# Kernel tuning notes

Measured on AMD Instinct MI355X. Metric: run time of the kernel, lower is better.

The kernel has to match this reference:

```python
import jax, jax.numpy as jnp
from jax import lax
import numpy as np

GRID, IMG, BLOCK = 60, 960, 16
BN_EPS = 1e-5


def _conv(x, w, b):
    return lax.conv_general_dilated(x, w, (1, 1), 'SAME', dimension_numbers=('NCHW', 'OIHW', 'NCHW')) + b[None, :, None, None]


def _bn(x, g, b):
    # inference BatchNorm with running_mean=0, running_var=1
    s = g * np.float32(1.0 / np.sqrt(1.0 + BN_EPS))
    return x * s[None, :, None, None] + b[None, :, None, None]


def _mlp(x, w1, b1, w2, b2):
    return jax.nn.relu(x @ w1.T + b1) @ w2.T + b2


def _lstm_layer(x, wih, whh, b):
    # x: [B,T,D]; torch gate order i,f,g,o; zero initial state
    B = x.shape[0]
    H = whh.shape[1]
    pre = jnp.swapaxes(x, 0, 1) @ wih.T + b  # [T,B,4H]

    def step(carry, p):
        h, c = carry
        z = p + h @ whh.T
        i, f, g, o = jnp.split(z, 4, axis=-1)
        c = jax.nn.sigmoid(f) * c + jax.nn.sigmoid(i) * jnp.tanh(g)
        h = jax.nn.sigmoid(o) * jnp.tanh(c)
        return (h, c), h

    z0 = jnp.zeros((B, H), x.dtype)
    (h, c), ys = lax.scan(step, (z0, z0), pre)
    return jnp.swapaxes(ys, 0, 1), h, c


def _forward(motion_vectors, boxes, track_ids, conv1_w, conv1_b, bn1_g, bn1_b, conv2_w, conv2_b, bn2_g, bn2_b, conv3_w, conv3_b, bn3_g, bn3_b, agg_w1, agg_b1, agg_w2, agg_b2, bx_w1, bx_b1, bx_w2, bx_b2, id_table, proj_w, proj_b, empty_slot, l0_wih, l0_whh, l0_b, l1_wih, l1_whh, l1_b, hb_w1, hb_b1, hb_w2, hb_b2, hc_w1, hc_b1, hc_w2, hc_b2, ht_w1, ht_b1, ht_w2, ht_b2):
    B = motion_vectors.shape[0]
    # ---- grid encoder (Conv-BN-ReLU x3) ----
    x = jax.nn.relu(_bn(_conv(motion_vectors, conv1_w, conv1_b), bn1_g, bn1_b))
    x = jax.nn.relu(_bn(_conv(x, conv2_w, conv2_b), bn2_g, bn2_b))
    gf = jax.nn.relu(_bn(_conv(x, conv3_w, conv3_b), bn3_g, bn3_b))  # [B,64,60,60]
    global_feat = gf.mean((-2, -1))  # AdaptiveAvgPool2d(1) -> [B,64]

    # ---- per-box motion statistics (vectorized masked reductions) ----
    bg = jnp.clip(boxes * (IMG / BLOCK), 0.0, GRID - 1e-6)  # grid coords
    ix1 = jnp.floor(bg[..., 0]); iy1 = jnp.floor(bg[..., 1])
    ix2 = jnp.maximum(ix1 + 1.0, jnp.ceil(bg[..., 2]))
    iy2 = jnp.maximum(iy1 + 1.0, jnp.ceil(bg[..., 3]))
    g = jnp.arange(GRID, dtype=bg.dtype)
    mx_ = (g >= ix1[..., None]) & (g < ix2[..., None])  # [B,N,60]
    my_ = (g >= iy1[..., None]) & (g < iy2[..., None])
    mask = my_[..., :, None] & mx_[..., None, :]  # [B,N,60,60]
    m = mask.astype(bg.dtype)
    cnt = m.sum((-2, -1))[..., None]  # [B,N,1], >= 1 by construction
    mv = motion_vectors  # [B,2,60,60]
    s1 = jnp.einsum('bnyx,bcyx->bnc', m, mv)
    s2 = jnp.einsum('bnyx,bcyx->bnc', m, mv * mv)
    mean = s1 / cnt
    var = (s2 - cnt * mean * mean) / jnp.maximum(cnt - 1.0, 1.0)  # unbiased, like torch .std()
    var_safe = jnp.where(cnt > 1.0, jnp.maximum(var, 1e-12), 1.0)
    std = jnp.where(cnt > 1.0, jnp.sqrt(var_safe), 0.0)
    BIG = jnp.asarray(1e9, bg.dtype)
    mn = jnp.min(jnp.where(mask[:, :, None], mv[:, None], BIG), axis=(-2, -1))   # [B,N,2]
    mx = jnp.max(jnp.where(mask[:, :, None], mv[:, None], -BIG), axis=(-2, -1))  # [B,N,2]
    stats = jnp.stack([mean[..., 0], mean[..., 1], std[..., 0], std[..., 1], mn[..., 0], mx[..., 0], mn[..., 1], mx[..., 1]], -1)  # [B,N,8]
    motion_emb = _mlp(stats, agg_w1, agg_b1, agg_w2, agg_b2)  # [B,N,64]

    # ---- slot initialization ----
    box_emb = _mlp(boxes, bx_w1, bx_b1, bx_w2, bx_b2)  # [B,N,64]
    id_emb = id_table[jnp.clip(track_ids, 0, 999)]  # [B,N,32]
    obj = jnp.concatenate([box_emb, id_emb, motion_emb], -1)  # [B,N,160]
    slots = obj @ proj_w.T + proj_b  # [B,300,128]; N == max_slots so no empty slots used

    # ---- 2-layer LSTM over the 300 slots (batch_first, eval -> no dropout) ----
    Ns = slots.shape[1]
    gexp = jnp.broadcast_to(global_feat[:, None, :], (B, Ns, global_feat.shape[-1]))
    lstm_in = jnp.concatenate([slots, gexp], -1)  # [B,300,192]
    y, h0, c0 = _lstm_layer(lstm_in, l0_wih, l0_whh, l0_b)
    y, h1, c1 = _lstm_layer(y, l1_wih, l1_whh, l1_b)  # [B,300,128]

    # ---- RT-DETR style heads ----
    pred_boxes = jax.nn.sigmoid(_mlp(y, hb_w1, hb_b1, hb_w2, hb_b2))  # [B,300,4]
    cls_logits = _mlp(y, hc_w1, hc_b1, hc_w2, hc_b2)  # [B,300,2]
    tid_logits = _mlp(y, ht_w1, ht_b1, ht_w2, ht_b2)  # [B,300,1000]
    h = jnp.stack([h0, h1])
    c = jnp.stack([c0, c1])
    return pred_boxes, cls_logits, tid_logits, h, c


def setup_inputs() -> dict:
    B, N = 32, 300
    key = jax.random.key(0)
    ks = iter(jax.random.split(key, 60))

    def w(*s):
        return jax.random.normal(next(ks), s, jnp.float32) * 0.05

    mv = jax.random.normal(next(ks), (B, 2, GRID, GRID), jnp.float32)
    bb = jax.random.uniform(next(ks), (B, N, 4), jnp.float32)
    boxes = jnp.concatenate([jnp.minimum(bb[..., :2], bb[..., 2:]), jnp.maximum(bb[..., :2], bb[..., 2:])], -1)
    track_ids = jax.random.randint(next(ks), (B, N), 0, 1000)
    return dict(
        motion_vectors=mv, boxes=boxes, track_ids=track_ids,
        conv1_w=w(32, 2, 3, 3), conv1_b=w(32), bn1_g=1.0 + w(32), bn1_b=w(32),
        conv2_w=w(64, 32, 3, 3), conv2_b=w(64), bn2_g=1.0 + w(64), bn2_b=w(64),
        conv3_w=w(64, 64, 3, 3), conv3_b=w(64), bn3_g=1.0 + w(64), bn3_b=w(64),
        agg_w1=w(32, 8), agg_b1=w(32), agg_w2=w(64, 32), agg_b2=w(64),
        bx_w1=w(32, 4), bx_b1=w(32), bx_w2=w(64, 32), bx_b2=w(64),
        id_table=w(1000, 32).at[0].set(0.0),
        proj_w=w(128, 160), proj_b=w(128), empty_slot=w(128),
        l0_wih=w(512, 192), l0_whh=w(512, 128), l0_b=w(512),
        l1_wih=w(512, 128), l1_whh=w(512, 128), l1_b=w(512),
        hb_w1=w(256, 128), hb_b1=w(256), hb_w2=w(4, 256), hb_b2=w(4),
        hc_w1=w(256, 128), hc_b1=w(256), hc_w2=w(2, 256), hc_b2=w(2),
        ht_w1=w(256, 128), ht_b1=w(256), ht_w2=w(1000, 256), ht_b2=w(1000))


def reference(motion_vectors, boxes, track_ids, conv1_w, conv1_b, bn1_g, bn1_b, conv2_w, conv2_b, bn2_g, bn2_b, conv3_w, conv3_b, bn3_g, bn3_b, agg_w1, agg_b1, agg_w2, agg_b2, bx_w1, bx_b1, bx_w2, bx_b2, id_table, proj_w, proj_b, empty_slot, l0_wih, l0_whh, l0_b, l1_wih, l1_whh, l1_b, hb_w1, hb_b1, hb_w2, hb_b2, hc_w1, hc_b1, hc_w2, hc_b2, ht_w1, ht_b1, ht_w2, ht_b2):
    return _forward(motion_vectors, boxes, track_ids, conv1_w, conv1_b, bn1_g, bn1_b, conv2_w, conv2_b, bn2_g, bn2_b, conv3_w, conv3_b, bn3_g, bn3_b, agg_w1, agg_b1, agg_w2, agg_b2, bx_w1, bx_b1, bx_w2, bx_b2, id_table, proj_w, proj_b, empty_slot, l0_wih, l0_whh, l0_b, l1_wih, l1_whh, l1_b, hb_w1, hb_b1, hb_w2, hb_b2, hc_w1, hc_b1, hc_w2, hc_b2, ht_w1, ht_b1, ht_w2, ht_b2)
```

## Files before the change

### kernel.cpp

```cpp
#include <hip/hip_runtime.h>
#include <hip/hip_bf16.h>
#include <math.h>

typedef unsigned short ushort_t;
typedef __attribute__((ext_vector_type(8))) short bf16x8;
typedef __attribute__((ext_vector_type(4))) float f32x4;

__device__ __forceinline__ float sigf(float x) {
  x = fminf(fmaxf(x, -30.f), 30.f);
  return 1.f / (1.f + __expf(-x));
}
__device__ __forceinline__ float sig2(float x) {
  return __builtin_amdgcn_rcpf(1.f + __expf(-x));
}
__device__ __forceinline__ float tanh2(float x) {
  return 1.f - 2.f * __builtin_amdgcn_rcpf(__expf(2.f * x) + 1.f);
}
__device__ __forceinline__ ushort_t f2bf(float x) {
  unsigned int b = __float_as_uint(x);
  unsigned int lsb = (b >> 16) & 1u;
  b += 0x7fffu + lsb;
  return (ushort_t)(b >> 16);
}
__device__ __forceinline__ float bf2f(ushort_t u) {
  return __uint_as_float(((unsigned int)u) << 16);
}

#define NPIX 3600
__device__ __forceinline__ int gperm(int rho) {
  return ((rho & 3) << 7) + (rho >> 2);
}

__global__ __launch_bounds__(256) void wprep_kernel(
    const float* __restrict__ conv2_w, const float* __restrict__ conv3_w,
    const float* __restrict__ wih0,
    const float* __restrict__ projW,
    const float* __restrict__ projb,
    const float* __restrict__ l0_b,
    const float* __restrict__ hbw1, const float* __restrict__ hcw1,
    const float* __restrict__ htw1, const float* __restrict__ htw2,
    const float* __restrict__ hbb1, const float* __restrict__ hcb1,
    const float* __restrict__ htb1, ushort_t* __restrict__ wc2,
    ushort_t* __restrict__ wc3, ushort_t* __restrict__ wAp,
    float* __restrict__ l0bp, ushort_t* __restrict__ whid,
    ushort_t* __restrict__ wt2, float* __restrict__ bhid) {
  int i = blockIdx.x * 256 + threadIdx.x;
  if (i < 18432) {
    int oc = i / 288, r = i % 288, kt = r / 32, ic = r % 32;
    wc2[i] = f2bf(conv2_w[((oc * 32 + ic) * 3 + kt / 3) * 3 + kt % 3]);
    return;
  }
  i -= 18432;
  if (i < 36864) {
    int oc = i / 576, r = i % 576, c = r / 288, r2 = r % 288;
    int kt = r2 / 32, icl = r2 % 32, ic = c * 32 + icl;
    wc3[i] = f2bf(conv3_w[((oc * 64 + ic) * 3 + kt / 3) * 3 + kt % 3]);
    return;
  }
  i -= 36864;
  if (i < 98304) {
    int n = i / 192, k = i % 192;
    int src = gperm(n);
    float a = 0.f;
    if (k < 160) {
      const float* wr = wih0 + src * 192;
      for (int j = 0; j < 128; ++j) a = fmaf(wr[j], projW[j * 160 + k], a);
    }
    wAp[i] = f2bf(a);
    return;
  }
  i -= 98304;
  if (i < 512) {
    int src = gperm(i);
    float a = l0_b[src];
    const float* wr = wih0 + src * 192;
    for (int j = 0; j < 128; ++j) a = fmaf(wr[j], projb[j], a);
    l0bp[i] = a;
    return;
  }
  i -= 512;
  if (i < 98304) {
    int row = i >> 7, c = i & 127;
    float v = (row < 256)   ? hbw1[row * 128 + c]
              : (row < 512) ? hcw1[(row - 256) * 128 + c]
                            : htw1[(row - 512) * 128 + c];
    whid[i] = f2bf(v);
    return;
  }
  i -= 98304;
  if (i < 256000) {
    wt2[i] = f2bf(htw2[i]);
    return;
  }
  i -= 256000;
  if (i < 768)
    bhid[i] = (i < 256) ? hbb1[i] : (i < 512) ? hcb1[i - 256] : htb1[i - 512];
}

__global__ __launch_bounds__(256) void gvec_kernel(
    const float* __restrict__ wih0, const float* __restrict__ gf,
    float* __restrict__ gvec) {
  int i = blockIdx.x * 256 + threadIdx.x;
  int b = i >> 9, n = i & 511;
  const float* wr = wih0 + gperm(n) * 192 + 128;
  const float* g = gf + b * 64;
  float a = 0.f;
#pragma unroll
  for (int k = 0; k < 64; ++k) a = fmaf(wr[k], g[k], a);
  gvec[i] = a * (1.f / 3600.f);
}

__global__ __launch_bounds__(256) void front_kernel(
    const float* __restrict__ mv, const float* __restrict__ c1w,
    const float* __restrict__ c1b, const float* __restrict__ bg1,
    const float* __restrict__ bb1, ushort_t* __restrict__ x1out,
    const float* __restrict__ boxes, const int* __restrict__ ids,
    const float* __restrict__ agg_w1, const float* __restrict__ agg_b1,
    const float* __restrict__ agg_w2, const float* __restrict__ agg_b2,
    const float* __restrict__ bx_w1, const float* __restrict__ bx_b1,
    const float* __restrict__ bx_w2, const float* __restrict__ bx_b2,
    const float* __restrict__ id_table, ushort_t* __restrict__ obj_out) {
  if (blockIdx.x < 14400) {
    int idx = blockIdx.x * 256 + threadIdx.x;
    int x = idx % 60;
    int y = (idx / 60) % 60;
    int oc = (idx / 3600) % 32;
    int b = idx / (3600 * 32);
    float acc = 0.f;
#pragma unroll
    for (int ic = 0; ic < 2; ++ic) {
      const float* src = mv + (b * 2 + ic) * NPIX;
      const float* wp = c1w + (oc * 2 + ic) * 9;
#pragma unroll
      for (int ky = 0; ky < 3; ++ky) {
        int gy = y + ky - 1;
        if (gy < 0 || gy >= 60) continue;
#pragma unroll
        for (int kx = 0; kx < 3; ++kx) {
          int gx = x + kx - 1;
          if (gx < 0 || gx >= 60) continue;
          acc = fmaf(src[gy * 60 + gx], wp[ky * 3 + kx], acc);
        }
      }
    }
    float s = bg1[oc] * rsqrtf(1.f + 1e-5f);
    float v = fmaf(acc, s, fmaf(c1b[oc], s, bb1[oc]));
    x1out[idx] = f2bf(fmaxf(v, 0.f));
    return;
  }
  __shared__ float obj[2][160];
  __shared__ float hm[2][32];
  __shared__ float hbx[2][32];
  __shared__ float stats[2][8];
  __shared__ float boxf[2][4];
  __shared__ float red[2][2][8];
  int h = threadIdx.x >> 7;
  int t = threadIdx.x & 127;
  int blk = (blockIdx.x - 14400) * 2 + h;
  int b = blk / 300;
  float bx0 = boxes[blk * 4 + 0], by0 = boxes[blk * 4 + 1];
  float bx1 = boxes[blk * 4 + 2], by1 = boxes[blk * 4 + 3];
  const float HI = (float)(60.0 - 1e-6);
  float gx1 = fminf(fmaxf(bx0 * 60.f, 0.f), HI);
  float gy1 = fminf(fmaxf(by0 * 60.f, 0.f), HI);
  float gx2 = fminf(fmaxf(bx1 * 60.f, 0.f), HI);
  float gy2 = fminf(fmaxf(by1 * 60.f, 0.f), HI);
  float fx1 = floorf(gx1), fy1 = floorf(gy1);
  float fx2 = fmaxf(fx1 + 1.f, ceilf(gx2));
  float fy2 = fmaxf(fy1 + 1.f, ceilf(gy2));
  int ix1 = (int)fx1, iy1 = (int)fy1, ix2 = (int)fx2, iy2 = (int)fy2;
  int w = ix2 - ix1, hgt = iy2 - iy1;
  int area = w * hgt;
  float s0 = 0.f, s1 = 0.f, q0 = 0.f, q1 = 0.f;
  float mn0 = 1e9f, mn1 = 1e9f, mx0 = -1e9f, mx1 = -1e9f;
  const float* mv0 = mv + b * 2 * NPIX;
  const float* mv1 = mv0 + NPIX;
  for (int i = t; i < area; i += 128) {
    int r = i / w, cc = i - r * w;
    int yy = iy1 + r, xx = ix1 + cc;
    float v0 = mv0[yy * 60 + xx];
    float v1 = mv1[yy * 60 + xx];
    s0 += v0; q0 += v0 * v0; mn0 = fminf(mn0, v0); mx0 = fmaxf(mx0, v0);
    s1 += v1; q1 += v1 * v1; mn1 = fminf(mn1, v1); mx1 = fmaxf(mx1, v1);
  }
#pragma unroll
  for (int off = 32; off; off >>= 1) {
    s0 += __shfl_down(s0, off); s1 += __shfl_down(s1, off);
    q0 += __shfl_down(q0, off); q1 += __shfl_down(q1, off);
    mn0 = fminf(mn0, __shfl_down(mn0, off));
    mn1 = fminf(mn1, __shfl_down(mn1, off));
    mx0 = fmaxf(mx0, __shfl_down(mx0, off));
    mx1 = fmaxf(mx1, __shfl_down(mx1, off));
// ... 179 lines not shown
    }
#pragma unroll
    for (int q = 0; q < 2; ++q) {
      int idx = q * 256 + tid;
      int row = idx >> 3, ch = idx & 7;
      int n = n0 + row;
      uint4 v = make_uint4(0, 0, 0, 0);
      if (n < N) v = *(const uint4*)(W + (size_t)n * K + kc * 64 + ch * 8);
      *(uint4*)(&Ws[row * 64 + ((ch * 8) ^ ((row & 7) << 3))]) = v;
    }
    __syncthreads();
#pragma unroll
    for (int ks = 0; ks < 2; ++ks) {
      bf16x8 bfr[2], afr[4];
#pragma unroll
      for (int ni = 0; ni < 2; ++ni) {
        int row = wn * 32 + ni * 16 + col;
        bfr[ni] = *(const bf16x8*)(
            &Ws[row * 64 + ((ks * 32 + kg * 8) ^ ((row & 7) << 3))]);
      }
#pragma unroll
      for (int mi = 0; mi < 4; ++mi) {
        int row = wm * 64 + mi * 16 + col;
        afr[mi] = *(const bf16x8*)(
            &As[row * 64 + ((ks * 32 + kg * 8) ^ ((row & 7) << 3))]);
      }
#pragma unroll
      for (int mi = 0; mi < 4; ++mi)
#pragma unroll
        for (int ni = 0; ni < 2; ++ni)
          acc[mi][ni] = __builtin_amdgcn_mfma_f32_16x16x32_bf16(
              afr[mi], bfr[ni], acc[mi][ni], 0, 0, 0);
    }
  }
#pragma unroll
  for (int ni = 0; ni < 2; ++ni) {
    int n = n0 + wn * 32 + ni * 16 + col;
    float bn = (n < N) ? bias[n] : 0.f;
#pragma unroll
    for (int mi = 0; mi < 4; ++mi) {
      int mbase = m0 + wm * 64 + mi * 16 + kg * 4;
#pragma unroll
      for (int r = 0; r < 4; ++r) {
        float v = acc[mi][ni][r] + bn;
        if (GVEC) v += gvec[((mbase + r) / 300) * 512 + n];
        if (ACT == 1) v = fmaxf(v, 0.f);
        if (n < N) {
          if (OBF16)
            ((ushort_t*)C)[(size_t)(mbase + r) * ldc + n] = f2bf(v);
          else
            ((float*)C)[(size_t)(mbase + r) * ldc + n] = v;
        }
      }
    }
  }
}

__global__ __launch_bounds__(256) void head_small_kernel(
    const ushort_t* __restrict__ hid, const float* __restrict__ wb2,
    const float* __restrict__ bb2, const float* __restrict__ wc2,
    const float* __restrict__ bc2, float* __restrict__ outB,
    float* __restrict__ outC) {
  int idx = blockIdx.x * 256 + threadIdx.x;
  int row = idx / 6, j = idx % 6;
  const ushort_t* h = hid + (size_t)row * 768 + (j < 4 ? 0 : 256);
  const float* wrow = (j < 4) ? wb2 + j * 256 : wc2 + (j - 4) * 256;
  float acc = (j < 4) ? bb2[j] : bc2[j - 4];
  for (int k = 0; k < 256; k += 8) {
    uint4 hv = *(const uint4*)(h + k);
    unsigned int ww[4] = {hv.x, hv.y, hv.z, hv.w};
#pragma unroll
    for (int q = 0; q < 4; ++q) {
      acc = fmaf(bf2f((ushort_t)(ww[q] & 0xffff)), wrow[k + 2 * q], acc);
      acc = fmaf(bf2f((ushort_t)(ww[q] >> 16)), wrow[k + 2 * q + 1], acc);
    }
  }
  float v = (j < 4) ? sigf(acc) : acc;
  if (j < 4) outB[row * 4 + j] = v;
  else outC[row * 2 + (j - 4)] = v;
}

#define LSTM_BAR() asm volatile("s_waitcnt lgkmcnt(0)\n\ts_barrier" ::: "memory")

__global__ __launch_bounds__(512) void lstm_fused_kernel(
    const float* __restrict__ pre0,
    const float* __restrict__ whh0,
    const float* __restrict__ wih1,
    const float* __restrict__ whh1,
    const float* __restrict__ b1,
    float* __restrict__ pre1,
    ushort_t* __restrict__ y0,
    ushort_t* __restrict__ y1,
    float* __restrict__ outH, float* __restrict__ outC,
    unsigned int* __restrict__ flags)
{
  __shared__ ushort_t h_lds[2][4][160];
  int tid = threadIdx.x;
  int w = tid >> 6, lane = tid & 63;
  int col = lane & 15, kg = lane >> 4;
  int bat = col & 3, q = col >> 2;
  int cell = (4 * w + q) * 4 + kg;

  if (blockIdx.x < 8) {
    int g = blockIdx.x;
    int b0 = g * 4;
    unsigned int* flagp = &flags[g * 32];
    for (int i = tid; i < 2 * 4 * 160; i += 512) ((ushort_t*)h_lds)[i] = 0;
    bf16x8 aW0[4][4];
#pragma unroll
    for (int j = 0; j < 4; ++j) {
      int rho = (4 * w + j) * 16 + col;
      int src = gperm(rho);
#pragma unroll
      for (int kt = 0; kt < 4; ++kt) {
        const float* s1 = whh0 + src * 128 + kt * 32 + kg * 8;
        bf16x8 f1;
#pragma unroll
        for (int qq = 0; qq < 8; ++qq) f1[qq] = (short)f2bf(s1[qq]);
        aW0[j][kt] = f1;
      }
    }
    const float* pg = pre0 + (size_t)(b0 + bat) * 300 * 512 + 4 * cell;
    ushort_t* yg0 = y0 + ((size_t)(b0 + bat) * 300) * 128 + cell;
    float c = 0.f, hout = 0.f;
    f32x4 p0v = *(const f32x4*)(pg);
    f32x4 p1v = *(const f32x4*)(pg + 512);
    __syncthreads();

    for (int s = 0; s < 300; ++s) {
      const ushort_t* hb = h_lds[s & 1][bat];
      bf16x8 bfr[4];
#pragma unroll
      for (int kt = 0; kt < 4; ++kt)
        bfr[kt] = *(const bf16x8*)(hb + kt * 32 + kg * 8);
      f32x4 a0 = {0.f, 0.f, 0.f, 0.f}, a1 = a0, a2 = a0, a3 = a0;
#pragma unroll
      for (int kt = 0; kt < 4; ++kt) {
        a0 = __builtin_amdgcn_mfma_f32_16x16x32_bf16(aW0[0][kt], bfr[kt], a0, 0, 0, 0);
        a1 = __builtin_amdgcn_mfma_f32_16x16x32_bf16(aW0[1][kt], bfr[kt], a1, 0, 0, 0);
        a2 = __builtin_amdgcn_mfma_f32_16x16x32_bf16(aW0[2][kt], bfr[kt], a2, 0, 0, 0);
        a3 = __builtin_amdgcn_mfma_f32_16x16x32_bf16(aW0[3][kt], bfr[kt], a3, 0, 0, 0);
      }
      f32x4 z = a0;
      if (q == 1) z = a1;
      if (q == 2) z = a2;
      if (q == 3) z = a3;
      {
        float zi = z[0] + p0v[0];
        float zf = z[1] + p0v[1];
        float zg = z[2] + p0v[2];
        float zo = z[3] + p0v[3];
        float vi = sig2(zi), vf = sig2(zf), vg = tanh2(zg), vo = sig2(zo);
        c = vf * c + vi * vg;
        hout = vo * tanh2(c);
        ushort_t hv = f2bf(hout);
        h_lds[(s + 1) & 1][bat][cell] = hv;
        __builtin_nontemporal_store(hv, yg0 + (size_t)s * 128);
        p0v = p1v;
        int sn = (s + 2 < 300) ? s + 2 : 299;
        p1v = *(const f32x4*)(pg + (size_t)sn * 512);
      }
      asm volatile("s_waitcnt vmcnt(6)" ::: "memory");
      LSTM_BAR();
      if (tid == 0 && s >= 3)
        __hip_atomic_store(flagp, (unsigned int)(s - 3), __ATOMIC_RELAXED,
                           __HIP_MEMORY_SCOPE_AGENT);
    }
    asm volatile("s_waitcnt vmcnt(0)" ::: "memory");
    __syncthreads();
    if (tid == 0)
      __hip_atomic_store(flagp, 300u, __ATOMIC_RELAXED,
                         __HIP_MEMORY_SCOPE_AGENT);
    outH[(b0 + bat) * 128 + cell] = hout;
    outC[(b0 + bat) * 128 + cell] = c;
  } else if (blockIdx.x < 16) {
    int g = blockIdx.x - 8;
    int b0 = g * 4;
    unsigned int* flagp = &flags[g * 32 + 16];
    for (int i = tid; i < 2 * 4 * 160; i += 512) ((ushort_t*)h_lds)[i] = 0;
    bf16x8 aW[4][4];
#pragma unroll
    for (int j = 0; j < 4; ++j) {
      int rho = (4 * w + j) * 16 + col;
      int src = gperm(rho);
#pragma unroll
      for (int kt = 0; kt < 4; ++kt) {
        const float* s1 = whh1 + src * 128 + kt * 32 + kg * 8;
        bf16x8 f1;
#pragma unroll
        for (int qq = 0; qq < 8; ++qq) f1[qq] = (short)f2bf(s1[qq]);
        aW[j][kt] = f1;
      }
    }
    float bi = b1[cell], bff = b1[128 + cell], bgg = b1[256 + cell],
          boo = b1[384 + cell];
    const float* pg = pre1 + (size_t)(b0 + bat) * 300 * 512 + 4 * cell;
    ushort_t* yg = y1 + (size_t)(b0 + bat) * 300 * 128 + cell;
    float c = 0.f, hout = 0.f;
    unsigned int fc = 0;
    f32x4 p0v, p1v;
    do {
      fc = __hip_atomic_load(flagp, __ATOMIC_RELAXED,
                             __HIP_MEMORY_SCOPE_AGENT);
      if (fc < 1) __builtin_amdgcn_s_sleep(2);
    } while (fc < 1);
    asm volatile("" ::: "memory");
    p0v = __builtin_nontemporal_load((const f32x4*)(pg));
    while (fc < 2) {
      fc = __hip_atomic_load(flagp, __ATOMIC_RELAXED,
                             __HIP_MEMORY_SCOPE_AGENT);
      if (fc < 2) __builtin_amdgcn_s_sleep(2);
    }
    asm volatile("" ::: "memory");
    p1v = __builtin_nontemporal_load((const f32x4*)(pg + 512));
    __syncthreads();

    for (int t = 0; t < 300; ++t) {
      const ushort_t* hb = h_lds[t & 1][bat];
      bf16x8 bfr[4];
#pragma unroll
      for (int kt = 0; kt < 4; ++kt)
        bfr[kt] = *(const bf16x8*)(hb + kt * 32 + kg * 8);
      f32x4 a0 = {0.f, 0.f, 0.f, 0.f}, a1 = a0, a2 = a0, a3 = a0;
#pragma unroll
      for (int kt = 0; kt < 4; ++kt) {
        a0 = __builtin_amdgcn_mfma_f32_16x16x32_bf16(aW[0][kt], bfr[kt], a0, 0, 0, 0);
        a1 = __builtin_amdgcn_mfma_f32_16x16x32_bf16(aW[1][kt], bfr[kt], a1, 0, 0, 0);
        a2 = __builtin_amdgcn_mfma_f32_16x16x32_bf16(aW[2][kt], bfr[kt], a2, 0, 0, 0);
        a3 = __builtin_amdgcn_mfma_f32_16x16x32_bf16(aW[3][kt], bfr[kt], a3, 0, 0, 0);
      }
      f32x4 z = a0;
      if (q == 1) z = a1;
      if (q == 2) z = a2;
      if (q == 3) z = a3;
      {
        float zi = z[0] + p0v[0] + bi;
        float zf = z[1] + p0v[1] + bff;
        float zg = z[2] + p0v[2] + bgg;
        float zo = z[3] + p0v[3] + boo;
        float vi = sig2(zi), vf = sig2(zf), vg = tanh2(zg), vo = sig2(zo);
        c = vf * c + vi * vg;
        hout = vo * tanh2(c);
        ushort_t hv = f2bf(hout);
        h_lds[(t + 1) & 1][bat][cell] = hv;
        yg[(size_t)t * 128] = hv;
        p0v = p1v;
        if (t + 2 < 300) {
          unsigned int need = (unsigned int)(t + 3);
          if (fc < need) {
            do {
              fc = __hip_atomic_load(flagp, __ATOMIC_RELAXED,
                                     __HIP_MEMORY_SCOPE_AGENT);
              if (fc < need) __builtin_amdgcn_s_sleep(2);
            } while (fc < need);
            asm volatile("" ::: "memory");
          }
          p1v = __builtin_nontemporal_load(
              (const f32x4*)(pg + (size_t)(t + 2) * 512));
        }
      }
      LSTM_BAR();
    }
    outH[4096 + (b0 + bat) * 128 + cell] = hout;
    outC[4096 + (b0 + bat) * 128 + cell] = c;
  } else {
    int g = blockIdx.x - 16;
    int b0 = g * 4;
    unsigned int* flag0 = &flags[g * 32];
    unsigned int* flag1 = &flags[g * 32 + 16];
    bf16x8 aU[4][4];
#pragma unroll
    for (int j = 0; j < 4; ++j) {
      int rho = (4 * w + j) * 16 + col;
      int src = gperm(rho);
#pragma unroll
      for (int kt = 0; kt < 4; ++kt) {
        const float* s2 = wih1 + src * 128 + kt * 32 + kg * 8;
        bf16x8 f2;
#pragma unroll
        for (int qq = 0; qq < 8; ++qq) f2[qq] = (short)f2bf(s2[qq]);
        aU[j][kt] = f2;
      }
    }
    int bb = col & 3;
    int ts = col >> 2;
    const ushort_t* yb = y0 + ((size_t)(b0 + bb) * 300) * 128 + kg * 8;
    unsigned int fc = 0;
    for (int t0 = 0; t0 < 300; t0 += 12) {
      unsigned int need = (unsigned int)(t0 + 11);
      while (fc < need) {
        fc = __hip_atomic_load(flag0, __ATOMIC_RELAXED,
                               __HIP_MEMORY_SCOPE_AGENT);
        if (fc < need) __builtin_amdgcn_s_sleep(2);
      }
      asm volatile("" ::: "memory");
      f32x4 acc[4][3];
#pragma unroll
      for (int j = 0; j < 4; ++j)
#pragma unroll
        for (int ct = 0; ct < 3; ++ct) acc[j][ct] = (f32x4){0.f, 0.f, 0.f, 0.f};
#pragma unroll
      for (int ct = 0; ct < 3; ++ct) {
        int t = t0 + ct * 4 + ts;
        bf16x8 bfr[4];
#pragma unroll
        for (int kt = 0; kt < 4; ++kt)
          bfr[kt] = __builtin_nontemporal_load(
              (const bf16x8*)(yb + (size_t)t * 128 + kt * 32));
#pragma unroll
        for (int kt = 0; kt < 4; ++kt) {
          acc[0][ct] = __builtin_amdgcn_mfma_f32_16x16x32_bf16(aU[0][kt], bfr[kt], acc[0][ct], 0, 0, 0);
          acc[1][ct] = __builtin_amdgcn_mfma_f32_16x16x32_bf16(aU[1][kt], bfr[kt], acc[1][ct], 0, 0, 0);
          acc[2][ct] = __builtin_amdgcn_mfma_f32_16x16x32_bf16(aU[2][kt], bfr[kt], acc[2][ct], 0, 0, 0);
          acc[3][ct] = __builtin_amdgcn_mfma_f32_16x16x32_bf16(aU[3][kt], bfr[kt], acc[3][ct], 0, 0, 0);
        }
      }
#pragma unroll
      for (int ct = 0; ct < 3; ++ct) {
        int t = t0 + ct * 4 + ts;
        float* pd = pre1 + ((size_t)(b0 + bb) * 300 + t) * 512 + kg * 4;
#pragma unroll
        for (int j = 0; j < 4; ++j)
          __builtin_nontemporal_store(acc[j][ct],
                                      (f32x4*)(pd + (4 * w + j) * 16));
      }
      asm volatile("s_waitcnt vmcnt(0)" ::: "memory");
      __syncthreads();
      if (tid == 0)
        __hip_atomic_store(flag1, (unsigned int)(t0 + 12), __ATOMIC_RELAXED,
                           __HIP_MEMORY_SCOPE_AGENT);
    }
  }
}

extern "C" void kernel_launch(void* const* d_in, const int* in_sizes, int n_in,
                              void* d_out, int out_size, void* d_ws,
                              size_t ws_size, hipStream_t stream) {
  const float* mv = (const float*)d_in[0];
  const float* boxes = (const float*)d_in[1];
  const int* track_ids = (const int*)d_in[2];
  const float* conv1_w = (const float*)d_in[3];
  const float* conv1_b = (const float*)d_in[4];
  const float* bn1_g = (const float*)d_in[5];
  const float* bn1_b = (const float*)d_in[6];
  const float* conv2_w = (const float*)d_in[7];
  const float* conv2_b = (const float*)d_in[8];
  const float* bn2_g = (const float*)d_in[9];
  const float* bn2_b = (const float*)d_in[10];
  const float* conv3_w = (const float*)d_in[11];
  const float* conv3_b = (const float*)d_in[12];
  const float* bn3_g = (const float*)d_in[13];
  const float* bn3_b = (const float*)d_in[14];
  const float* agg_w1 = (const float*)d_in[15];
  const float* agg_b1 = (const float*)d_in[16];
  const float* agg_w2 = (const float*)d_in[17];
  const float* agg_b2 = (const float*)d_in[18];
  const float* bx_w1 = (const float*)d_in[19];
  const float* bx_b1 = (const float*)d_in[20];
  const float* bx_w2 = (const float*)d_in[21];
  const float* bx_b2 = (const float*)d_in[22];
  const float* id_table = (const float*)d_in[23];
  const float* proj_w = (const float*)d_in[24];
  const float* proj_b = (const float*)d_in[25];
  const float* l0_wih = (const float*)d_in[27];
  const float* l0_whh = (const float*)d_in[28];
  const float* l0_b = (const float*)d_in[29];
  const float* l1_wih = (const float*)d_in[30];
  const float* l1_whh = (const float*)d_in[31];
  const float* l1_b = (const float*)d_in[32];
  const float* hb_w1 = (const float*)d_in[33];
  const float* hb_b1 = (const float*)d_in[34];
  const float* hb_w2 = (const float*)d_in[35];
  const float* hb_b2 = (const float*)d_in[36];
  const float* hc_w1 = (const float*)d_in[37];
  const float* hc_b1 = (const float*)d_in[38];
  const float* hc_w2 = (const float*)d_in[39];
  const float* hc_b2 = (const float*)d_in[40];
  const float* ht_w1 = (const float*)d_in[41];
  const float* ht_b1 = (const float*)d_in[42];
  const float* ht_w2 = (const float*)d_in[43];
  const float* ht_b2 = (const float*)d_in[44];

  char* wsb = (char*)d_ws;
  ushort_t* x1u = (ushort_t*)(wsb + 0);
  ushort_t* x2u = (ushort_t*)(wsb + 7372800);
  float* pre0 = (float*)(wsb + 0);
  ushort_t* hid = (ushort_t*)(wsb + 0);
  ushort_t* y0g = (ushort_t*)(wsb + 19660800);
  float* gf = (float*)(wsb + 22118400);
  ushort_t* obj = (ushort_t*)(wsb + 22126592);
  float* pre1 = (float*)(wsb + 25812992);
  ushort_t* y1b = (ushort_t*)(wsb + 45473792);
  unsigned int* flags = (unsigned int*)(wsb + 47931392);
  ushort_t* wAp = (ushort_t*)(wsb + 47932416);
  ushort_t* whid = (ushort_t*)(wsb + 48129024);
  ushort_t* wt2 = (ushort_t*)(wsb + 48325632);
  float* bhid = (float*)(wsb + 48837632);
  float* l0bp = (float*)(wsb + 48840704);
  float* gvec = (float*)(wsb + 48842752);
  ushort_t* wc2 = (ushort_t*)(wsb + 48908288);
  ushort_t* wc3 = (ushort_t*)(wsb + 48945152);

  float* outB = (float*)d_out;
  float* outC = outB + 38400;
  float* outT = outB + 57600;
  float* outH = outB + 9657600;
  float* outCc = outB + 9665792;

  hipMemsetAsync(gf, 0, 2048 * sizeof(float), stream);
  hipMemsetAsync(flags, 0, 1024, stream);

  wprep_kernel<<<1989, 256, 0, stream>>>(
      conv2_w, conv3_w, l0_wih, proj_w, proj_b, l0_b, hb_w1, hc_w1, ht_w1,
      ht_w2, hb_b1, hc_b1, ht_b1, wc2, wc3, wAp, l0bp, whid, wt2, bhid);
  front_kernel<<<19200, 256, 0, stream>>>(
      mv, conv1_w, conv1_b, bn1_g, bn1_b, x1u, boxes, track_ids, agg_w1,
      agg_b1, agg_w2, agg_b2, bx_w1, bx_b1, bx_w2, bx_b2, id_table, obj);
  conv_mfma_kernel<32, false><<<dim3(16, 32), 256, 0, stream>>>(
      x1u, wc2, conv2_b, bn2_g, bn2_b, x2u, nullptr);
  conv_mfma_kernel<64, true><<<dim3(16, 32), 256, 0, stream>>>(
      x2u, wc3, conv3_b, bn3_g, bn3_b, nullptr, gf);
  gvec_kernel<<<64, 256, 0, stream>>>(l0_wih, gf, gvec);
  gemm_bf16w_kernel<0, false, true><<<dim3(75, 8), 256, 0, stream>>>(
      obj, 192, wAp, l0bp, pre0, 512, 9600, 512, 192, gvec);
  lstm_fused_kernel<<<24, 512, 0, stream>>>(pre0, l0_whh, l1_wih, l1_whh,
                                            l1_b, pre1, y0g, y1b, outH, outCc,
                                            flags);
  gemm_bf16w_kernel<1, true, false><<<dim3(75, 12), 256, 0, stream>>>(
      y1b, 128, whid, bhid, hid, 768, 9600, 768, 128, nullptr);
  head_small_kernel<<<225, 256, 0, stream>>>(hid, hb_w2, hb_b2, hc_w2, hc_b2,
                                             outB, outC);
  gemm_bf16w_kernel<0, false, false><<<dim3(75, 16), 256, 0, stream>>>(
      hid + 512, 768, wt2, ht_b2, outT, 1000, 9600, 1000, 256, nullptr);
}
```

Baseline: 535.5 us.

## Halve LSTM block to four waves with two cells per lane and exp2-prescaled gates

The fused LSTM kernel now runs 256 threads per block instead of 512. Each wave holds 8 gate-weight tiles and each lane updates two hidden cells, so the per-step barrier spans fewer waves. Gate pre-activations are pre-multiplied by log2(e), or 2·log2(e) for the g gate, in the weight prep, bias and gvec kernels and in the recurrent weights, which lets the activations use exp2 directly without a multiply. In exchange each wave carries twice the register load and issues twice the MFMAs serially per step, which could lengthen the recurrent critical path.

```diff
diff --git a/kernel.cpp b/kernel.cpp
--- a/kernel.cpp
+++ b/kernel.cpp
@@ -6,15 +6,11 @@
 typedef __attribute__((ext_vector_type(8))) short bf16x8;
 typedef __attribute__((ext_vector_type(4))) float f32x4;
 
+#define LOG2E 1.4426950408889634f
+
 __device__ __forceinline__ float sigf(float x) {
   x = fminf(fmaxf(x, -30.f), 30.f);
   return 1.f / (1.f + __expf(-x));
-}
-__device__ __forceinline__ float sig2(float x) {
-  return __builtin_amdgcn_rcpf(1.f + __expf(-x));
-}
-__device__ __forceinline__ float tanh2(float x) {
-  return 1.f - 2.f * __builtin_amdgcn_rcpf(__expf(2.f * x) + 1.f);
 }
 __device__ __forceinline__ ushort_t f2bf(float x) {
   unsigned int b = __float_as_uint(x);
@@ -24,6 +20,9 @@
 }
 __device__ __forceinline__ float bf2f(ushort_t u) {
   return __uint_as_float(((unsigned int)u) << 16);
+}
+__device__ __forceinline__ float gsc(int g3) {
+  return (g3 == 2) ? (2.f * LOG2E) : LOG2E;
 }
 
 #define NPIX 3600
@@ -66,7 +65,7 @@
       const float* wr = wih0 + src * 192;
       for (int j = 0; j < 128; ++j) a = fmaf(wr[j], projW[j * 160 + k], a);
     }
-    wAp[i] = f2bf(a);
+    wAp[i] = f2bf(a * gsc(n & 3));
     return;
   }
   i -= 98304;
@@ -75,7 +74,7 @@
     float a = l0_b[src];
     const float* wr = wih0 + src * 192;
     for (int j = 0; j < 128; ++j) a = fmaf(wr[j], projb[j], a);
-    l0bp[i] = a;
+    l0bp[i] = a * gsc(i & 3);
     return;
   }
   i -= 512;
@@ -107,7 +106,7 @@
   float a = 0.f;
 #pragma unroll
   for (int k = 0; k < 64; ++k) a = fmaf(wr[k], g[k], a);
-  gvec[i] = a * (1.f / 3600.f);
+  gvec[i] = a * (1.f / 3600.f) * gsc(n & 3);
 }
 
 __global__ __launch_bounds__(256) void front_kernel(
@@ -453,7 +452,7 @@
 
 #define LSTM_BAR() asm volatile("s_waitcnt lgkmcnt(0)\n\ts_barrier" ::: "memory")
 
-__global__ __launch_bounds__(512) void lstm_fused_kernel(
+__global__ __launch_bounds__(256, 1) void lstm_fused_kernel(
     const float* __restrict__ pre0,
     const float* __restrict__ whh0,
     const float* __restrict__ wih1,
@@ -470,32 +469,38 @@
   int w = tid >> 6, lane = tid & 63;
   int col = lane & 15, kg = lane >> 4;
   int bat = col & 3, q = col >> 2;
-  int cell = (4 * w + q) * 4 + kg;
+  int cellA = 32 * w + 4 * q + kg;
+  int cellB = cellA + 16;
+  float wsc = gsc(col & 3);
 
   if (blockIdx.x < 8) {
     int g = blockIdx.x;
     int b0 = g * 4;
     unsigned int* flagp = &flags[g * 32];
-    for (int i = tid; i < 2 * 4 * 160; i += 512) ((ushort_t*)h_lds)[i] = 0;
-    bf16x8 aW0[4][4];
-#pragma unroll
-    for (int j = 0; j < 4; ++j) {
-      int rho = (4 * w + j) * 16 + col;
+    for (int i = tid; i < 2 * 4 * 160; i += 256) ((ushort_t*)h_lds)[i] = 0;
+    bf16x8 aW0[8][4];
+#pragma unroll
+    for (int j = 0; j < 8; ++j) {
+      int rho = (8 * w + j) * 16 + col;
       int src = gperm(rho);
 #pragma unroll
       for (int kt = 0; kt < 4; ++kt) {
         const float* s1 = whh0 + src * 128 + kt * 32 + kg * 8;
         bf16x8 f1;
 #pragma unroll
-        for (int qq = 0; qq < 8; ++qq) f1[qq] = (short)f2bf(s1[qq]);
+        for (int qq = 0; qq < 8; ++qq) f1[qq] = (short)f2bf(s1[qq] * wsc);
         aW0[j][kt] = f1;
       }
     }
-    const float* pg = pre0 + (size_t)(b0 + bat) * 300 * 512 + 4 * cell;
-    ushort_t* yg0 = y0 + ((size_t)(b0 + bat) * 300) * 128 + cell;
-    float c = 0.f, hout = 0.f;
-    f32x4 p0v = *(const f32x4*)(pg);
-    f32x4 p1v = *(const f32x4*)(pg + 512);
+    const float* pgA = pre0 + (size_t)(b0 + bat) * 300 * 512 + 4 * cellA;
+    const float* pgB = pgA + 64;
+    ushort_t* ygA = y0 + ((size_t)(b0 + bat) * 300) * 128 + cellA;
+    ushort_t* ygB = ygA + 16;
+    float cA = 0.f, cB = 0.f, hA = 0.f, hB = 0.f;
+    f32x4 p0A = *(const f32x4*)(pgA);
+    f32x4 p0B = *(const f32x4*)(pgB);
+    f32x4 p1A = *(const f32x4*)(pgA + 512);
+    f32x4 p1B = *(const f32x4*)(pgB + 512);
     __syncthreads();
 
     for (int s = 0; s < 300; ++s) {
@@ -504,34 +509,61 @@
 #pragma unroll
       for (int kt = 0; kt < 4; ++kt)
         bfr[kt] = *(const bf16x8*)(hb + kt * 32 + kg * 8);
-      f32x4 a0 = {0.f, 0.f, 0.f, 0.f}, a1 = a0, a2 = a0, a3 = a0;
+      f32x4 ac0 = {0.f, 0.f, 0.f, 0.f}, ac1 = ac0, ac2 = ac0, ac3 = ac0;
+      f32x4 ac4 = ac0, ac5 = ac0, ac6 = ac0, ac7 = ac0;
 #pragma unroll
       for (int kt = 0; kt < 4; ++kt) {
-        a0 = __builtin_amdgcn_mfma_f32_16x16x32_bf16(aW0[0][kt], bfr[kt], a0, 0, 0, 0);
-        a1 = __builtin_amdgcn_mfma_f32_16x16x32_bf16(aW0[1][kt], bfr[kt], a1, 0, 0, 0);
-        a2 = __builtin_amdgcn_mfma_f32_16x16x32_bf16(aW0[2][kt], bfr[kt], a2, 0, 0, 0);
-        a3 = __builtin_amdgcn_mfma_f32_16x16x32_bf16(aW0[3][kt], bfr[kt], a3, 0, 0, 0);
-      }
-      f32x4 z = a0;
-      if (q == 1) z = a1;
-      if (q == 2) z = a2;
-      if (q == 3) z = a3;
+        ac0 = __builtin_amdgcn_mfma_f32_16x16x32_bf16(aW0[0][kt], bfr[kt], ac0, 0, 0, 0);
+        ac1 = __builtin_amdgcn_mfma_f32_16x16x32_bf16(aW0[1][kt], bfr[kt], ac1, 0, 0, 0);
+        ac2 = __builtin_amdgcn_mfma_f32_16x16x32_bf16(aW0[2][kt], bfr[kt], ac2, 0, 0, 0);
+        ac3 = __builtin_amdgcn_mfma_f32_16x16x32_bf16(aW0[3][kt], bfr[kt], ac3, 0, 0, 0);
+        ac4 = __builtin_amdgcn_mfma_f32_16x16x32_bf16(aW0[4][kt], bfr[kt], ac4, 0, 0, 0);
+        ac5 = __builtin_amdgcn_mfma_f32_16x16x32_bf16(aW0[5][kt], bfr[kt], ac5, 0, 0, 0);
+        ac6 = __builtin_amdgcn_mfma_f32_16x16x32_bf16(aW0[6][kt], bfr[kt], ac6, 0, 0, 0);
+        ac7 = __builtin_amdgcn_mfma_f32_16x16x32_bf16(aW0[7][kt], bfr[kt], ac7, 0, 0, 0);
+      }
+      f32x4 zA = ac0;
+      if (q == 1) zA = ac1;
+      if (q == 2) zA = ac2;
+      if (q == 3) zA = ac3;
+      f32x4 zB = ac4;
+      if (q == 1) zB = ac5;
+      if (q == 2) zB = ac6;
+      if (q == 3) zB = ac7;
       {
-        float zi = z[0] + p0v[0];
-        float zf = z[1] + p0v[1];
-        float zg = z[2] + p0v[2];
-        float zo = z[3] + p0v[3];
-        float vi = sig2(zi), vf = sig2(zf), vg = tanh2(zg), vo = sig2(zo);
-        c = vf * c + vi * vg;
-        hout = vo * tanh2(c);
-        ushort_t hv = f2bf(hout);
-        h_lds[(s + 1) & 1][bat][cell] = hv;
-        __builtin_nontemporal_store(hv, yg0 + (size_t)s * 128);
-        p0v = p1v;
-        int sn = (s + 2 < 300) ? s + 2 : 299;
-        p1v = *(const f32x4*)(pg + (size_t)sn * 512);
-      }
-      asm volatile("s_waitcnt vmcnt(6)" ::: "memory");
+        float zi = zA[0] + p0A[0], zf = zA[1] + p0A[1];
+        float zg = zA[2] + p0A[2], zo = zA[3] + p0A[3];
+        float vi = __builtin_amdgcn_rcpf(1.f + __builtin_amdgcn_exp2f(-zi));
+        float vf = __builtin_amdgcn_rcpf(1.f + __builtin_amdgcn_exp2f(-zf));
+        float vg = 1.f - 2.f * __builtin_amdgcn_rcpf(__builtin_amdgcn_exp2f(zg) + 1.f);
+        float vo = __builtin_amdgcn_rcpf(1.f + __builtin_amdgcn_exp2f(-zo));
+        cA = vf * cA + vi * vg;
+        hA = vo * (1.f - 2.f * __builtin_amdgcn_rcpf(
+                             __builtin_amdgcn_exp2f(2.f * LOG2E * cA) + 1.f));
+        ushort_t hv = f2bf(hA);
+        h_lds[(s + 1) & 1][bat][cellA] = hv;
+        __builtin_nontemporal_store(hv, ygA + (size_t)s * 128);
+      }
+      {
+        float zi = zB[0] + p0B[0], zf = zB[1] + p0B[1];
+        float zg = zB[2] + p0B[2], zo = zB[3] + p0B[3];
+        float vi = __builtin_amdgcn_rcpf(1.f + __builtin_amdgcn_exp2f(-zi));
+        float vf = __builtin_amdgcn_rcpf(1.f + __builtin_amdgcn_exp2f(-zf));
+        float vg = 1.f - 2.f * __builtin_amdgcn_rcpf(__builtin_amdgcn_exp2f(zg) + 1.f);
+        float vo = __builtin_amdgcn_rcpf(1.f + __builtin_amdgcn_exp2f(-zo));
+        cB = vf * cB + vi * vg;
+        hB = vo * (1.f - 2.f * __builtin_amdgcn_rcpf(
+                             __builtin_amdgcn_exp2f(2.f * LOG2E * cB) + 1.f));
+        ushort_t hv = f2bf(hB);
+        h_lds[(s + 1) & 1][bat][cellB] = hv;
+        __builtin_nontemporal_store(hv, ygB + (size_t)s * 128);
+      }
+      p0A = p1A;
+      p0B = p1B;
+      int sn = (s + 2 < 300) ? s + 2 : 299;
+      p1A = *(const f32x4*)(pgA + (size_t)sn * 512);
+      p1B = *(const f32x4*)(pgB + (size_t)sn * 512);
+      asm volatile("s_waitcnt vmcnt(12)" ::: "memory");
       LSTM_BAR();
       if (tid == 0 && s >= 3)
         __hip_atomic_store(flagp, (unsigned int)(s - 3), __ATOMIC_RELAXED,
@@ -542,48 +574,56 @@
     if (tid == 0)
       __hip_atomic_store(flagp, 300u, __ATOMIC_RELAXED,
                          __HIP_MEMORY_SCOPE_AGENT);
-    outH[(b0 + bat) * 128 + cell] = hout;
-    outC[(b0 + bat) * 128 + cell] = c;
+    outH[(b0 + bat) * 128 + cellA] = hA;
+    outH[(b0 + bat) * 128 + cellB] = hB;
+    outC[(b0 + bat) * 128 + cellA] = cA;
+    outC[(b0 + bat) * 128 + cellB] = cB;
   } else if (blockIdx.x < 16) {
     int g = blockIdx.x - 8;
     int b0 = g * 4;
     unsigned int* flagp = &flags[g * 32 + 16];
-    for (int i = tid; i < 2 * 4 * 160; i += 512) ((ushort_t*)h_lds)[i] = 0;
-    bf16x8 aW[4][4];
-#pragma unroll
-    for (int j = 0; j < 4; ++j) {
-      int rho = (4 * w + j) * 16 + col;
+    for (int i = tid; i < 2 * 4 * 160; i += 256) ((ushort_t*)h_lds)[i] = 0;
+    bf16x8 aW[8][4];
+#pragma unroll
+    for (int j = 0; j < 8; ++j) {
+      int rho = (8 * w + j) * 16 + col;
       int src = gperm(rho);
 #pragma unroll
       for (int kt = 0; kt < 4; ++kt) {
         const float* s1 = whh1 + src * 128 + kt * 32 + kg * 8;
         bf16x8 f1;
 #pragma unroll
-        for (int qq = 0; qq < 8; ++qq) f1[qq] = (short)f2bf(s1[qq]);
+        for (int qq = 0; qq < 8; ++qq) f1[qq] = (short)f2bf(s1[qq] * wsc);
         aW[j][kt] = f1;
       }
     }
-    float bi = b1[cell], bff = b1[128 + cell], bgg = b1[256 + cell],
-          boo = b1[384 + cell];
-    const float* pg = pre1 + (size_t)(b0 + bat) * 300 * 512 + 4 * cell;
-    ushort_t* yg = y1 + (size_t)(b0 + bat) * 300 * 128 + cell;
-    float c = 0.f, hout = 0.f;
+    float biA = b1[cellA] * LOG2E, bfA = b1[128 + cellA] * LOG2E;
+    float bgA = b1[256 + cellA] * (2.f * LOG2E), boA = b1[384 + cellA] * LOG2E;
+    float biB = b1[cellB] * LOG2E, bfB = b1[128 + cellB] * LOG2E;
+    float bgB = b1[256 + cellB] * (2.f * LOG2E), boB = b1[384 + cellB] * LOG2E;
+    const float* pgA = pre1 + (size_t)(b0 + bat) * 300 * 512 + 4 * cellA;
+    const float* pgB = pgA + 64;
+    ushort_t* ygA = y1 + (size_t)(b0 + bat) * 300 * 128 + cellA;
+    ushort_t* ygB = ygA + 16;
+    float cA = 0.f, cB = 0.f, hA = 0.f, hB = 0.f;
     unsigned int fc = 0;
-    f32x4 p0v, p1v;
+    f32x4 p0A, p0B, p1A, p1B;
     do {
       fc = __hip_atomic_load(flagp, __ATOMIC_RELAXED,
                              __HIP_MEMORY_SCOPE_AGENT);
       if (fc < 1) __builtin_amdgcn_s_sleep(2);
     } while (fc < 1);
     asm volatile("" ::: "memory");
-    p0v = __builtin_nontemporal_load((const f32x4*)(pg));
+    p0A = __builtin_nontemporal_load((const f32x4*)(pgA));
+    p0B = __builtin_nontemporal_load((const f32x4*)(pgB));
     while (fc < 2) {
       fc = __hip_atomic_load(flagp, __ATOMIC_RELAXED,
                              __HIP_MEMORY_SCOPE_AGENT);
       if (fc < 2) __builtin_amdgcn_s_sleep(2);
     }
     asm volatile("" ::: "memory");
-    p1v = __builtin_nontemporal_load((const f32x4*)(pg + 512));
+    p1A = __builtin_nontemporal_load((const f32x4*)(pgA + 512));
+    p1B = __builtin_nontemporal_load((const f32x4*)(pgB + 512));
     __syncthreads();
 
     for (int t = 0; t < 300; ++t) {
@@ -592,64 +632,94 @@
 #pragma unroll
       for (int kt = 0; kt < 4; ++kt)
         bfr[kt] = *(const bf16x8*)(hb + kt * 32 + kg * 8);
-      f32x4 a0 = {0.f, 0.f, 0.f, 0.f}, a1 = a0, a2 = a0, a3 = a0;
+      f32x4 ac0 = {0.f, 0.f, 0.f, 0.f}, ac1 = ac0, ac2 = ac0, ac3 = ac0;
+      f32x4 ac4 = ac0, ac5 = ac0, ac6 = ac0, ac7 = ac0;
 #pragma unroll
       for (int kt = 0; kt < 4; ++kt) {
-        a0 = __builtin_amdgcn_mfma_f32_16x16x32_bf16(aW[0][kt], bfr[kt], a0, 0, 0, 0);
-        a1 = __builtin_amdgcn_mfma_f32_16x16x32_bf16(aW[1][kt], bfr[kt], a1, 0, 0, 0);
-        a2 = __builtin_amdgcn_mfma_f32_16x16x32_bf16(aW[2][kt], bfr[kt], a2, 0, 0, 0);
-        a3 = __builtin_amdgcn_mfma_f32_16x16x32_bf16(aW[3][kt], bfr[kt], a3, 0, 0, 0);
-      }
-      f32x4 z = a0;
-      if (q == 1) z = a1;
-      if (q == 2) z = a2;
-      if (q == 3) z = a3;
+        ac0 = __builtin_amdgcn_mfma_f32_16x16x32_bf16(aW[0][kt], bfr[kt], ac0, 0, 0, 0);
+        ac1 = __builtin_amdgcn_mfma_f32_16x16x32_bf16(aW[1][kt], bfr[kt], ac1, 0, 0, 0);
+        ac2 = __builtin_amdgcn_mfma_f32_16x16x32_bf16(aW[2][kt], bfr[kt], ac2, 0, 0, 0);
+        ac3 = __builtin_amdgcn_mfma_f32_16x16x32_bf16(aW[3][kt], bfr[kt], ac3, 0, 0, 0);
+        ac4 = __builtin_amdgcn_mfma_f32_16x16x32_bf16(aW[4][kt], bfr[kt], ac4, 0, 0, 0);
+        ac5 = __builtin_amdgcn_mfma_f32_16x16x32_bf16(aW[5][kt], bfr[kt], ac5, 0, 0, 0);
+        ac6 = __builtin_amdgcn_mfma_f32_16x16x32_bf16(aW[6][kt], bfr[kt], ac6, 0, 0, 0);
+        ac7 = __builtin_amdgcn_mfma_f32_16x16x32_bf16(aW[7][kt], bfr[kt], ac7, 0, 0, 0);
+      }
+      f32x4 zA = ac0;
+      if (q == 1) zA = ac1;
+      if (q == 2) zA = ac2;
+      if (q == 3) zA = ac3;
+      f32x4 zB = ac4;
+      if (q == 1) zB = ac5;
+      if (q == 2) zB = ac6;
+      if (q == 3) zB = ac7;
       {
-        float zi = z[0] + p0v[0] + bi;
-        float zf = z[1] + p0v[1] + bff;
-        float zg = z[2] + p0v[2] + bgg;
-        float zo = z[3] + p0v[3] + boo;
-        float vi = sig2(zi), vf = sig2(zf), vg = tanh2(zg), vo = sig2(zo);
-        c = vf * c + vi * vg;
-        hout = vo * tanh2(c);
-        ushort_t hv = f2bf(hout);
-        h_lds[(t + 1) & 1][bat][cell] = hv;
-        yg[(size_t)t * 128] = hv;
-        p0v = p1v;
-        if (t + 2 < 300) {
-          unsigned int need = (unsigned int)(t + 3);
-          if (fc < need) {
-            do {
-              fc = __hip_atomic_load(flagp, __ATOMIC_RELAXED,
-                                     __HIP_MEMORY_SCOPE_AGENT);
-              if (fc < need) __builtin_amdgcn_s_sleep(2);
-            } while (fc < need);
-            asm volatile("" ::: "memory");
-          }
-          p1v = __builtin_nontemporal_load(
-              (const f32x4*)(pg + (size_t)(t + 2) * 512));
+        float zi = zA[0] + p0A[0] + biA, zf = zA[1] + p0A[1] + bfA;
+        float zg = zA[2] + p0A[2] + bgA, zo = zA[3] + p0A[3] + boA;
+        float vi = __builtin_amdgcn_rcpf(1.f + __builtin_amdgcn_exp2f(-zi));
+        float vf = __builtin_amdgcn_rcpf(1.f + __builtin_amdgcn_exp2f(-zf));
+        float vg = 1.f - 2.f * __builtin_amdgcn_rcpf(__builtin_amdgcn_exp2f(zg) + 1.f);
+        float vo = __builtin_amdgcn_rcpf(1.f + __builtin_amdgcn_exp2f(-zo));
+        cA = vf * cA + vi * vg;
+        hA = vo * (1.f - 2.f * __builtin_amdgcn_rcpf(
+                             __builtin_amdgcn_exp2f(2.f * LOG2E * cA) + 1.f));
+        ushort_t hv = f2bf(hA);
+        h_lds[(t + 1) & 1][bat][cellA] = hv;
+        ygA[(size_t)t * 128] = hv;
+      }
+      {
+        float zi = zB[0] + p0B[0] + biB, zf = zB[1] + p0B[1] + bfB;
+        float zg = zB[2] + p0B[2] + bgB, zo = zB[3] + p0B[3] + boB;
+        float vi = __builtin_amdgcn_rcpf(1.f + __builtin_amdgcn_exp2f(-zi));
+        float vf = __builtin_amdgcn_rcpf(1.f + __builtin_amdgcn_exp2f(-zf));
+        float vg = 1.f - 2.f * __builtin_amdgcn_rcpf(__builtin_amdgcn_exp2f(zg) + 1.f);
+        float vo = __builtin_amdgcn_rcpf(1.f + __builtin_amdgcn_exp2f(-zo));
+        cB = vf * cB + vi * vg;
+        hB = vo * (1.f - 2.f * __builtin_amdgcn_rcpf(
+                             __builtin_amdgcn_exp2f(2.f * LOG2E * cB) + 1.f));
+        ushort_t hv = f2bf(hB);
+        h_lds[(t + 1) & 1][bat][cellB] = hv;
+        ygB[(size_t)t * 128] = hv;
+      }
+      p0A = p1A;
+      p0B = p1B;
+      if (t + 2 < 300) {
+        unsigned int need = (unsigned int)(t + 3);
+        if (fc < need) {
+          do {
+            fc = __hip_atomic_load(flagp, __ATOMIC_RELAXED,
+                                   __HIP_MEMORY_SCOPE_AGENT);
+            if (fc < need) __builtin_amdgcn_s_sleep(2);
+          } while (fc < need);
+          asm volatile("" ::: "memory");
         }
+        p1A = __builtin_nontemporal_load(
+            (const f32x4*)(pgA + (size_t)(t + 2) * 512));
+        p1B = __builtin_nontemporal_load(
+            (const f32x4*)(pgB + (size_t)(t + 2) * 512));
       }
       LSTM_BAR();
     }
-    outH[4096 + (b0 + bat) * 128 + cell] = hout;
-    outC[4096 + (b0 + bat) * 128 + cell] = c;
+    outH[4096 + (b0 + bat) * 128 + cellA] = hA;
+    outH[4096 + (b0 + bat) * 128 + cellB] = hB;
+    outC[4096 + (b0 + bat) * 128 + cellA] = cA;
+    outC[4096 + (b0 + bat) * 128 + cellB] = cB;
   } else {
     int g = blockIdx.x - 16;
     int b0 = g * 4;
     unsigned int* flag0 = &flags[g * 32];
     unsigned int* flag1 = &flags[g * 32 + 16];
-    bf16x8 aU[4][4];
-#pragma unroll
-    for (int j = 0; j < 4; ++j) {
-      int rho = (4 * w + j) * 16 + col;
+    bf16x8 aU[8][4];
+#pragma unroll
+    for (int j = 0; j < 8; ++j) {
+      int rho = (8 * w + j) * 16 + col;
       int src = gperm(rho);
 #pragma unroll
       for (int kt = 0; kt < 4; ++kt) {
         const float* s2 = wih1 + src * 128 + kt * 32 + kg * 8;
         bf16x8 f2;
 #pragma unroll
-        for (int qq = 0; qq < 8; ++qq) f2[qq] = (short)f2bf(s2[qq]);
+        for (int qq = 0; qq < 8; ++qq) f2[qq] = (short)f2bf(s2[qq] * wsc);
         aU[j][kt] = f2;
       }
     }
@@ -665,11 +735,6 @@
         if (fc < need) __builtin_amdgcn_s_sleep(2);
       }
       asm volatile("" ::: "memory");
-      f32x4 acc[4][3];
-#pragma unroll
-      for (int j = 0; j < 4; ++j)
-#pragma unroll
-        for (int ct = 0; ct < 3; ++ct) acc[j][ct] = (f32x4){0.f, 0.f, 0.f, 0.f};
 #pragma unroll
       for (int ct = 0; ct < 3; ++ct) {
         int t = t0 + ct * 4 + ts;
@@ -678,22 +743,28 @@
         for (int kt = 0; kt < 4; ++kt)
           bfr[kt] = __builtin_nontemporal_load(
               (const bf16x8*)(yb + (size_t)t * 128 + kt * 32));
+        f32x4 u0 = {0.f, 0.f, 0.f, 0.f}, u1 = u0, u2 = u0, u3 = u0;
+        f32x4 u4 = u0, u5 = u0, u6 = u0, u7 = u0;
 #pragma unroll
         for (int kt = 0; kt < 4; ++kt) {
-          acc[0][ct] = __builtin_amdgcn_mfma_f32_16x16x32_bf16(aU[0][kt], bfr[kt], acc[0][ct], 0, 0, 0);
-          acc[1][ct] = __builtin_amdgcn_mfma_f32_16x16x32_bf16(aU[1][kt], bfr[kt], acc[1][ct], 0, 0, 0);
-          acc[2][ct] = __builtin_amdgcn_mfma_f32_16x16x32_bf16(aU[2][kt], bfr[kt], acc[2][ct], 0, 0, 0);
-          acc[3][ct] = __builtin_amdgcn_mfma_f32_16x16x32_bf16(aU[3][kt], bfr[kt], acc[3][ct], 0, 0, 0);
+          u0 = __builtin_amdgcn_mfma_f32_16x16x32_bf16(aU[0][kt], bfr[kt], u0, 0, 0, 0);
+          u1 = __builtin_amdgcn_mfma_f32_16x16x32_bf16(aU[1][kt], bfr[kt], u1, 0, 0, 0);
+          u2 = __builtin_amdgcn_mfma_f32_16x16x32_bf16(aU[2][kt], bfr[kt], u2, 0, 0, 0);
+          u3 = __builtin_amdgcn_mfma_f32_16x16x32_bf16(aU[3][kt], bfr[kt], u3, 0, 0, 0);
+          u4 = __builtin_amdgcn_mfma_f32_16x16x32_bf16(aU[4][kt], bfr[kt], u4, 0, 0, 0);
+          u5 = __builtin_amdgcn_mfma_f32_16x16x32_bf16(aU[5][kt], bfr[kt], u5, 0, 0, 0);
+          u6 = __builtin_amdgcn_mfma_f32_16x16x32_bf16(aU[6][kt], bfr[kt], u6, 0, 0, 0);
+          u7 = __builtin_amdgcn_mfma_f32_16x16x32_bf16(aU[7][kt], bfr[kt], u7, 0, 0, 0);
         }
-      }
-#pragma unroll
-      for (int ct = 0; ct < 3; ++ct) {
-        int t = t0 + ct * 4 + ts;
         float* pd = pre1 + ((size_t)(b0 + bb) * 300 + t) * 512 + kg * 4;
-#pragma unroll
-        for (int j = 0; j < 4; ++j)
-          __builtin_nontemporal_store(acc[j][ct],
-                                      (f32x4*)(pd + (4 * w + j) * 16));
+        __builtin_nontemporal_store(u0, (f32x4*)(pd + (8 * w + 0) * 16));
+        __builtin_nontemporal_store(u1, (f32x4*)(pd + (8 * w + 1) * 16));
+        __builtin_nontemporal_store(u2, (f32x4*)(pd + (8 * w + 2) * 16));
+        __builtin_nontemporal_store(u3, (f32x4*)(pd + (8 * w + 3) * 16));
+        __builtin_nontemporal_store(u4, (f32x4*)(pd + (8 * w + 4) * 16));
+        __builtin_nontemporal_store(u5, (f32x4*)(pd + (8 * w + 5) * 16));
+        __builtin_nontemporal_store(u6, (f32x4*)(pd + (8 * w + 6) * 16));
+        __builtin_nontemporal_store(u7, (f32x4*)(pd + (8 * w + 7) * 16));
       }
       asm volatile("s_waitcnt vmcnt(0)" ::: "memory");
       __syncthreads();
@@ -794,7 +865,7 @@
   gvec_kernel<<<64, 256, 0, stream>>>(l0_wih, gf, gvec);
   gemm_bf16w_kernel<0, false, true><<<dim3(75, 8), 256, 0, stream>>>(
       obj, 192, wAp, l0bp, pre0, 512, 9600, 512, 192, gvec);
-  lstm_fused_kernel<<<24, 512, 0, stream>>>(pre0, l0_whh, l1_wih, l1_whh,
+  lstm_fused_kernel<<<24, 256, 0, stream>>>(pre0, l0_whh, l1_wih, l1_whh,
                                             l1_b, pre1, y0g, y1b, outH, outCc,
                                             flags);
   gemm_bf16w_kernel<1, true, false><<<dim3(75, 12), 256, 0, stream>>>(
```

Measured after the change: 580.0 us. 1.08x slower.
